# Optimization experiments

Measured on AMD Instinct MI355X. Metric: run time of the kernel, lower is better.

## Reference

```python
import jax, jax.numpy as jnp
import numpy as np

N_GRAPHS = 1000  # fixed num_segments (torch uses batch.max()+1; ids drawn in [0, N_GRAPHS))


def setup_inputs() -> dict:
    key = jax.random.key(0)
    ks = jax.random.split(key, 12)
    n, d, h, e = 100000, 128, 128, 1600000
    x = jax.random.normal(ks[0], (n, d), jnp.float32)
    edge_index = jax.random.randint(ks[1], (2, e), 0, n)
    batch = jnp.sort(jax.random.randint(ks[2], (n,), 0, N_GRAPHS))

    def lin_w(k, i, o):
        return jax.random.normal(k, (i, o), jnp.float32) / np.sqrt(i).astype(np.float32)

    return {
        "x": x, "edge_index": edge_index, "batch": batch,
        "W0": lin_w(ks[3], d, h), "b0": jnp.zeros((h,), jnp.float32),
        "W1": lin_w(ks[4], h, h), "b1": jnp.zeros((h,), jnp.float32),
        "W2": lin_w(ks[5], h, h), "b2": jnp.zeros((h,), jnp.float32),
        "Wp1": lin_w(ks[6], h, h), "bp1": jnp.zeros((h,), jnp.float32),
        "Wp2": lin_w(ks[7], h, 1), "bp2": jnp.zeros((1,), jnp.float32),
    }


def reference(x, edge_index, batch, W0, b0, W1, b1, W2, b2, Wp1, bp1, Wp2, bp2):
    n = x.shape[0]
    src, dst = edge_index[0], edge_index[1]
    loop = jnp.arange(n, dtype=edge_index.dtype)
    src_a = jnp.concatenate([src, loop])  # [E+N]
    dst_a = jnp.concatenate([dst, loop])  # [E+N]

    # degree with self-loops, symmetric GCN norm per edge
    deg = jax.ops.segment_sum(jnp.ones_like(dst_a, dtype=x.dtype), dst_a, num_segments=n)
    dd = deg[src_a] * deg[dst_a]
    norm = jnp.where(dd > 0, jax.lax.rsqrt(dd), jnp.zeros_like(dd))  # [E+N]

    for W, b in ((W0, b0), (W1, b1), (W2, b2)):
        h = x @ W + b                              # [N, H] dense linear
        msg = h[src_a] * norm[:, None]             # gather + scale, [E+N, H]
        out = jax.ops.segment_sum(msg, dst_a, num_segments=n)  # scatter-add
        x = jax.nn.relu(out)

    # segment-mean pool over graphs
    pool = jax.ops.segment_sum(x, batch, num_segments=N_GRAPHS)  # [G, H]
    cnt = jax.ops.segment_sum(jnp.ones((n,), x.dtype), batch, num_segments=N_GRAPHS)
    pool = pool / jnp.clip(cnt, 1.0)[:, None]

    hid = jax.nn.relu(pool @ Wp1 + bp1)
    return (hid @ Wp2 + bp2).squeeze(-1)  # [G]
```

## Files before the change

kernel.cpp:

```cpp
#include <hip/hip_runtime.h>
#include <hip/hip_bf16.h>
#include <math.h>


typedef float f32x4 __attribute__((ext_vector_type(4)));
typedef short s16x8 __attribute__((ext_vector_type(8)));
typedef _Float16 f16;
typedef _Float16 f16x4 __attribute__((ext_vector_type(4)));

__device__ __forceinline__ unsigned short f2bf(float x) {
  unsigned u = __float_as_uint(x);
  unsigned r = (u + 0x7FFFu + ((u >> 16) & 1u)) >> 16;
  return (unsigned short)r;
}

__global__ __launch_bounds__(1024) void tile_reduce_kernel(
    const int* __restrict__ indeg, int* __restrict__ tilesum, int n) {
  __shared__ int ws[16];
  int i = blockIdx.x * 1024 + threadIdx.x;
  int v = (i < n) ? indeg[i] : 0;
  for (int off = 32; off > 0; off >>= 1) v += __shfl_down(v, off);
  int wid = threadIdx.x >> 6, lane = threadIdx.x & 63;
  if (lane == 0) ws[wid] = v;
  __syncthreads();
  if (threadIdx.x == 0) {
    int s = 0;
    for (int w = 0; w < 16; ++w) s += ws[w];
    tilesum[blockIdx.x] = s;
  }
}

__global__ __launch_bounds__(1024) void scan_emit_kernel(
    const int* __restrict__ indeg, const int* __restrict__ tilesum,
    int* __restrict__ ptr, float* __restrict__ rsq, int n, int T) {
  __shared__ int wsum[16];
  __shared__ int tilebase_s;
  int bid = blockIdx.x;
  int lane = threadIdx.x & 63, wid = threadIdx.x >> 6;
  if (threadIdx.x < 64) {
    int acc = 0;
    for (int t = threadIdx.x; t < bid; t += 64) acc += tilesum[t];
    for (int off = 32; off > 0; off >>= 1) acc += __shfl_down(acc, off);
    if (threadIdx.x == 0) tilebase_s = acc;
  }
  __syncthreads();
  int tilebase = tilebase_s;
  int i = bid * 1024 + threadIdx.x;
  int v = (i < n) ? indeg[i] : 0;
  int x = v;
  for (int off = 1; off < 64; off <<= 1) {
    int y = __shfl_up(x, off);
    if (lane >= off) x += y;
  }
  if (lane == 63) wsum[wid] = x;
  __syncthreads();
  if (threadIdx.x == 0) {
    int run = 0;
    for (int w = 0; w < 16; ++w) { int t = wsum[w]; wsum[w] = run; run += t; }
  }
  __syncthreads();
  if (i < n) {
    ptr[i] = x - v + wsum[wid] + tilebase;
    rsq[i] = 1.0f / sqrtf((float)(v + 1));
  }
  if (bid == T - 1 && threadIdx.x == 1023) ptr[n] = tilebase + wsum[15] + x;
}

__device__ __forceinline__ void wsplit_body(
    int blk, const float* __restrict__ W0, const float* __restrict__ W1,
    const float* __restrict__ W2, short* __restrict__ Whi, short* __restrict__ Wlo) {
  int layer = blk >> 6;
  int i = (blk & 63) * 256 + threadIdx.x;
  const float* W = (layer == 0) ? W0 : (layer == 1) ? W1 : W2;
  int j = i & 7, lane = (i >> 3) & 63, ks = (i >> 9) & 3, nt = i >> 11;
  int k = ks * 32 + (lane >> 4) * 8 + j;
  int nn = nt * 16 + (lane & 15);
  float w = W[k * 128 + nn];
  unsigned short h = f2bf(w);
  float hf = __uint_as_float(((unsigned)h) << 16);
  Whi[layer * 16384 + i] = (short)h;
  Wlo[layer * 16384 + i] = (short)f2bf(w - hf);
}

__global__ __launch_bounds__(256) void uber0_kernel(
    const int* __restrict__ dst, int* __restrict__ indeg, int* __restrict__ rank,
    int E,
    const float* __restrict__ W0, const float* __restrict__ W1,
    const float* __restrict__ W2, short* __restrict__ Whi, short* __restrict__ Wlo,
    const int* __restrict__ batch, int* __restrict__ gptr, int n, int G,
    float* __restrict__ pool, int CD, int GBD) {
  int b = blockIdx.x;
  if (b < CD) {
    int e = b * 256 + threadIdx.x;
    if (e < E) rank[e] = atomicAdd(&indeg[dst[e]], 1);
  } else if (b < CD + 192) {
    wsplit_body(b - CD, W0, W1, W2, Whi, Wlo);
  } else if (b < CD + 192 + GBD) {
    int i = (b - CD - 192) * 256 + threadIdx.x;
    if (i < n) {
      int bb = batch[i];
      if (i == 0) {
        for (int g = 0; g <= bb; ++g) gptr[g] = 0;
      } else {
        int bp = batch[i - 1];
        for (int g = bp + 1; g <= bb; ++g) gptr[g] = i;
      }
      if (i == n - 1) {
        for (int g = bb + 1; g <= G; ++g) gptr[g] = n;
      }
    }
  } else {
    int i = (b - CD - 192 - GBD) * 256 + threadIdx.x;
    if (i * 4 < G * 128) ((float4*)pool)[i] = make_float4(0.f, 0.f, 0.f, 0.f);
  }
}

__global__ void fill_all_kernel(const int* __restrict__ src, const int* __restrict__ dst,
                                const int* __restrict__ rank, const int* __restrict__ ptr,
                                int* __restrict__ csrc, int E) {
  int i = blockIdx.x * 256 + threadIdx.x;
  if (i < E) {
    int s = src[i], d = dst[i], r = rank[i];
    csrc[ptr[d] + r] = s;
  }
}

__global__ __launch_bounds__(256) void gemm1_kernel(
    const float* __restrict__ X, const short* __restrict__ Whi,
    const short* __restrict__ Wlo, const float* __restrict__ bias,
    const float* __restrict__ rsq, f16* __restrict__ H, int n) {
  int wave = threadIdx.x >> 6, lane = threadIdx.x & 63;
  int quad = lane >> 4, m = lane & 15;
  int mbase = blockIdx.x * 64 + wave * 16;
  int row = min(mbase + m, n - 1);
  const float* xr = X + (size_t)row * 128 + quad * 8;
  const s16x8* WH = (const s16x8*)Whi;
  const s16x8* WL = (const s16x8*)Wlo;
  f32x4 acc[8];
#pragma unroll
  for (int nt = 0; nt < 8; ++nt) acc[nt] = 0.f;
#pragma unroll
  for (int ks = 0; ks < 4; ++ks) {
    float4 xa = *(const float4*)(xr + ks * 32);
    float4 xb = *(const float4*)(xr + ks * 32 + 4);
    float xs[8] = {xa.x, xa.y, xa.z, xa.w, xb.x, xb.y, xb.z, xb.w};
    s16x8 ah, al;
#pragma unroll
    for (int j = 0; j < 8; ++j) {
      unsigned short h = f2bf(xs[j]);
      float hf = __uint_as_float(((unsigned)h) << 16);
      ah[j] = (short)h;
      al[j] = (short)f2bf(xs[j] - hf);
    }
#pragma unroll
    for (int nt = 0; nt < 8; ++nt) {
      s16x8 wh = WH[(nt * 4 + ks) * 64 + lane];
      s16x8 wl = WL[(nt * 4 + ks) * 64 + lane];
      acc[nt] = __builtin_amdgcn_mfma_f32_16x16x32_bf16(ah, wh, acc[nt], 0, 0, 0);
      acc[nt] = __builtin_amdgcn_mfma_f32_16x16x32_bf16(al, wh, acc[nt], 0, 0, 0);
      acc[nt] = __builtin_amdgcn_mfma_f32_16x16x32_bf16(ah, wl, acc[nt], 0, 0, 0);
    }
  }
  float rs[4];
#pragma unroll
  for (int r = 0; r < 4; ++r) {
    int rr = mbase + quad * 4 + r;
    rs[r] = (rr < n) ? rsq[rr] : 0.f;
  }
#pragma unroll
  for (int nt = 0; nt < 8; ++nt) {
    int col = nt * 16 + m;
    float b = bias[col];
#pragma unroll
    for (int r = 0; r < 4; ++r) {
      int rr = mbase + quad * 4 + r;
      if (rr < n) H[(size_t)rr * 128 + col] = (f16)((acc[nt][r] + b) * rs[r]);
    }
  }
}

__device__ __forceinline__ f32x4 agg_sum(
    const f16* __restrict__ H, const int* __restrict__ ptr,
    const int* __restrict__ csrc, int node, int hl) {
  const char* Hb = (const char*)H;
  unsigned hoff = (unsigned)hl << 3;
  int beg = ptr[node], end = ptr[node + 1];
  f32x4 a = __builtin_convertvector(
      *(const f16x4*)(Hb + (((unsigned)node << 8) | hoff)), f32x4);
#define ROW(s) (*(const f16x4*)(Hb + (((unsigned)(s) << 8) + hoff)))
  for (int base = beg; base < end; base += 32) {
    int m = end - base;
    if (m > 32) m = 32;
    int sl = (hl < m) ? csrc[base + hl] : 0;
    int j = 0;
    for (; j + 15 < m; j += 16) {
      int s0 = __shfl(sl, j + 0, 32), s1 = __shfl(sl, j + 1, 32);
      int s2 = __shfl(sl, j + 2, 32), s3 = __shfl(sl, j + 3, 32);
      int s4 = __shfl(sl, j + 4, 32), s5 = __shfl(sl, j + 5, 32);
      int s6 = __shfl(sl, j + 6, 32), s7 = __shfl(sl, j + 7, 32);
      int s8 = __shfl(sl, j + 8, 32), s9 = __shfl(sl, j + 9, 32);
      int sa = __shfl(sl, j + 10, 32), sb = __shfl(sl, j + 11, 32);
      int sc = __shfl(sl, j + 12, 32), sd = __shfl(sl, j + 13, 32);
      int se = __shfl(sl, j + 14, 32), sf = __shfl(sl, j + 15, 32);
      f16x4 h0 = ROW(s0), h1 = ROW(s1), h2 = ROW(s2), h3 = ROW(s3);
      f16x4 h4 = ROW(s4), h5 = ROW(s5), h6 = ROW(s6), h7 = ROW(s7);
      f16x4 h8 = ROW(s8), h9 = ROW(s9), ha = ROW(sa), hb = ROW(sb);
      f16x4 hc = ROW(sc), hd = ROW(sd), he = ROW(se), hf = ROW(sf);
      f16x4 t0 = ((h0 + h1) + (h2 + h3)) + ((h4 + h5) + (h6 + h7));
      f16x4 t1 = ((h8 + h9) + (ha + hb)) + ((hc + hd) + (he + hf));
      a += __builtin_convertvector(t0, f32x4);
      a += __builtin_convertvector(t1, f32x4);
    }
    for (; j + 7 < m; j += 8) {
      int s0 = __shfl(sl, j + 0, 32), s1 = __shfl(sl, j + 1, 32);
      int s2 = __shfl(sl, j + 2, 32), s3 = __shfl(sl, j + 3, 32);
      int s4 = __shfl(sl, j + 4, 32), s5 = __shfl(sl, j + 5, 32);
      int s6 = __shfl(sl, j + 6, 32), s7 = __shfl(sl, j + 7, 32);
      f16x4 h0 = ROW(s0), h1 = ROW(s1), h2 = ROW(s2), h3 = ROW(s3);
      f16x4 h4 = ROW(s4), h5 = ROW(s5), h6 = ROW(s6), h7 = ROW(s7);
      f16x4 t0 = ((h0 + h1) + (h2 + h3)) + ((h4 + h5) + (h6 + h7));
      a += __builtin_convertvector(t0, f32x4);
    }
    for (; j + 3 < m; j += 4) {
      int s0 = __shfl(sl, j + 0, 32), s1 = __shfl(sl, j + 1, 32);
      int s2 = __shfl(sl, j + 2, 32), s3 = __shfl(sl, j + 3, 32);
      f16x4 t0 = (ROW(s0) + ROW(s1)) + (ROW(s2) + ROW(s3));
      a += __builtin_convertvector(t0, f32x4);
    }
    for (; j < m; ++j) {
      int s0 = __shfl(sl, j, 32);
      a += __builtin_convertvector(ROW(s0), f32x4);
    }
  }
#undef ROW
  return a;
}

#define LDS_STRIDE 132
__global__ __launch_bounds__(256) void agg_gemm_kernel(
    const f16* __restrict__ H, const int* __restrict__ ptr,
    const int* __restrict__ csrc, const float* __restrict__ rsq,
    const short* __restrict__ Whi, const short* __restrict__ Wlo,
    const float* __restrict__ bias, f16* __restrict__ Hout, int n) {
  __shared__ int lds[16 * LDS_STRIDE];
  int hw = threadIdx.x >> 5, hl = threadIdx.x & 31;
  int nbase = blockIdx.x * 16;
#pragma unroll
  for (int rep = 0; rep < 2; ++rep) {
    int nl = hw + rep * 8;
    int node = nbase + nl;
    f32x4 o = 0.f;
    if (node < n) {
      f32x4 s = agg_sum(H, ptr, csrc, node, hl);
      float r = rsq[node];
      o.x = fmaxf(s.x * r, 0.f);
      o.y = fmaxf(s.y * r, 0.f);
      o.z = fmaxf(s.z * r, 0.f);
      o.w = fmaxf(s.w * r, 0.f);
    }
    int* dst = lds + nl * LDS_STRIDE + hl * 4;
#pragma unroll
    for (int c = 0; c < 4; ++c) {
      float v = o[c];
      unsigned short h = f2bf(v);
      float hf = __uint_as_float(((unsigned)h) << 16);
      unsigned short l = f2bf(v - hf);
      dst[c] = (int)((((unsigned)h) << 16) | l);
    }
  }
  __syncthreads();

  int wave = threadIdx.x >> 6, lane = threadIdx.x & 63;
  int quad = lane >> 4, m = lane & 15;
  const s16x8* WH = (const s16x8*)Whi;
  const s16x8* WL = (const s16x8*)Wlo;
  f32x4 acc0 = 0.f, acc1 = 0.f;
  int nt0 = wave * 2, nt1 = wave * 2 + 1;
#pragma unroll
  for (int ks = 0; ks < 4; ++ks) {
    const int* arow = lds + m * LDS_STRIDE + ks * 32 + quad * 8;
    s16x8 ah, al;
#pragma unroll
    for (int j = 0; j < 8; ++j) {
      unsigned p = (unsigned)arow[j];
      ah[j] = (short)(p >> 16);
      al[j] = (short)(p & 0xffffu);
    }
    s16x8 wh0 = WH[(nt0 * 4 + ks) * 64 + lane];
    s16x8 wl0 = WL[(nt0 * 4 + ks) * 64 + lane];
    s16x8 wh1 = WH[(nt1 * 4 + ks) * 64 + lane];
    s16x8 wl1 = WL[(nt1 * 4 + ks) * 64 + lane];
    acc0 = __builtin_amdgcn_mfma_f32_16x16x32_bf16(ah, wh0, acc0, 0, 0, 0);
    acc0 = __builtin_amdgcn_mfma_f32_16x16x32_bf16(al, wh0, acc0, 0, 0, 0);
    acc0 = __builtin_amdgcn_mfma_f32_16x16x32_bf16(ah, wl0, acc0, 0, 0, 0);
    acc1 = __builtin_amdgcn_mfma_f32_16x16x32_bf16(ah, wh1, acc1, 0, 0, 0);
    acc1 = __builtin_amdgcn_mfma_f32_16x16x32_bf16(al, wh1, acc1, 0, 0, 0);
    acc1 = __builtin_amdgcn_mfma_f32_16x16x32_bf16(ah, wl1, acc1, 0, 0, 0);
  }
  float rs[4];
#pragma unroll
  for (int r = 0; r < 4; ++r) {
    int rr = nbase + quad * 4 + r;
    rs[r] = (rr < n) ? rsq[rr] : 0.f;
  }
#pragma unroll
  for (int t = 0; t < 2; ++t) {
    int nt = wave * 2 + t;
    int col = nt * 16 + m;
    float b = bias[col];
    f32x4 a = t ? acc1 : acc0;
#pragma unroll
    for (int r = 0; r < 4; ++r) {
      int rr = nbase + quad * 4 + r;
      if (rr < n) Hout[(size_t)rr * 128 + col] = (f16)((a[r] + b) * rs[r]);
    }
  }
}

__global__ __launch_bounds__(256) void agg_pool_kernel(
    const f16* __restrict__ H, const int* __restrict__ ptr,
    const int* __restrict__ csrc, const float* __restrict__ rsq,
    const int* __restrict__ batch, float* __restrict__ pool, int n) {
  __shared__ float rows[16][128];
  __shared__ int gids[16];
  int hw = threadIdx.x >> 5, hl = threadIdx.x & 31;
  int nbase = blockIdx.x * 16;
#pragma unroll
  for (int rep = 0; rep < 2; ++rep) {
    int nl = hw + rep * 8;
    int node = nbase + nl;
    f32x4 o = 0.f;
    if (node < n) {
      f32x4 s = agg_sum(H, ptr, csrc, node, hl);
      float r = rsq[node];
      o.x = fmaxf(s.x * r, 0.f);
      o.y = fmaxf(s.y * r, 0.f);
      o.z = fmaxf(s.z * r, 0.f);
      o.w = fmaxf(s.w * r, 0.f);
    }
    *(f32x4*)&rows[nl][hl * 4] = o;
    if (hl == 0) gids[nl] = (node < n) ? batch[node] : -1;
  }
  __syncthreads();
  int half = threadIdx.x >> 7;
  int ch = threadIdx.x & 127;
  float acc = 0.f;
  int curg = gids[half * 8];
  for (int i = half * 8; i < half * 8 + 8; ++i) {
    int g = gids[i];
    if (g != curg) {
      if (curg >= 0) atomicAdd(&pool[(size_t)curg * 128 + ch], acc);
      acc = 0.f;
      curg = g;
    }
    if (g >= 0) acc += rows[i][ch];
  }
  if (curg >= 0) atomicAdd(&pool[(size_t)curg * 128 + ch], acc);
}

__global__ __launch_bounds__(128) void head_kernel(
    const float* __restrict__ pool, const int* __restrict__ gptr,
    const float* __restrict__ Wp1, const float* __restrict__ bp1,
    const float* __restrict__ Wp2, const float* __restrict__ bp2,
    float* __restrict__ out, int G) {
  int g = blockIdx.x;
  int j = threadIdx.x;
  __shared__ float ps[128];
  __shared__ float hs[128];
  int cnt = gptr[g + 1] - gptr[g];
  float inv = 1.0f / (float)max(cnt, 1);
  ps[j] = pool[(size_t)g * 128 + j] * inv;
  __syncthreads();
  float acc = bp1[j];
#pragma unroll 8
  for (int k = 0; k < 128; ++k) acc = fmaf(ps[k], Wp1[k * 128 + j], acc);
  hs[j] = fmaxf(acc, 0.f) * Wp2[j];
  __syncthreads();
  for (int off = 64; off > 0; off >>= 1) {
    if (j < off) hs[j] += hs[j + off];
    __syncthreads();
  }
  if (j == 0) out[g] = hs[0] + bp2[0];
}

extern "C" void kernel_launch(void* const* d_in, const int* in_sizes, int n_in,
                              void* d_out, int out_size, void* d_ws, size_t ws_size,
                              hipStream_t stream) {
  const float* x    = (const float*)d_in[0];
  const int*   eidx = (const int*)d_in[1];
  const int*   batch= (const int*)d_in[2];
  const float* W0 = (const float*)d_in[3];
  const float* b0 = (const float*)d_in[4];
  const float* W1 = (const float*)d_in[5];
  const float* b1 = (const float*)d_in[6];
  const float* W2 = (const float*)d_in[7];
  const float* b2 = (const float*)d_in[8];
  const float* Wp1 = (const float*)d_in[9];
  const float* bp1 = (const float*)d_in[10];
  const float* Wp2 = (const float*)d_in[11];
  const float* bp2 = (const float*)d_in[12];
  float* out = (float*)d_out;

  const int N = in_sizes[0] / 128;
  const int E = in_sizes[1] / 2;
  const int G = out_size;
  const int T = (N + 1023) / 1024;

  const int* src = eidx;
  const int* dst = eidx + E;

  char* ws = (char*)d_ws;
  size_t off = 0;
  auto alloc = [&](size_t bytes) -> void* {
    void* p = ws + off;
    off = (off + bytes + 255) & ~(size_t)255;
    return p;
  };
  int*   indeg   = (int*)  alloc((size_t)N * 4);
  int*   ptr     = (int*)  alloc((size_t)(N + 1) * 4);
  float* rsq     = (float*)alloc((size_t)N * 4);
  int*   rank    = (int*)  alloc((size_t)E * 4);
  int*   csrc    = (int*)  alloc((size_t)E * 4);
  f16*   bufA    = (f16*)  alloc((size_t)N * 128 * 2);
  f16*   bufB    = (f16*)  alloc((size_t)N * 128 * 2);
  int*   gptr    = (int*)  alloc((size_t)(G + 1) * 4);
  float* pool    = (float*)alloc((size_t)G * 128 * 4);
  int*   tilesum = (int*)  alloc((size_t)T * 4);
  short* whi     = (short*)alloc(3 * 16384 * 2);
  short* wlo     = (short*)alloc(3 * 16384 * 2);
  (void)ws_size;

  hipMemsetAsync(indeg, 0, (size_t)N * 4, stream);

  const int CD  = (E + 255) / 256;
  const int GBD = (N + 255) / 256;
  const int PZ  = (G * 128 / 4 + 255) / 256;
  uber0_kernel<<<CD + 192 + GBD + PZ, 256, 0, stream>>>(
      dst, indeg, rank, E, W0, W1, W2, whi, wlo, batch, gptr, N, G, pool,
      CD, GBD);

  tile_reduce_kernel<<<T, 1024, 0, stream>>>(indeg, tilesum, N);
  scan_emit_kernel<<<T, 1024, 0, stream>>>(indeg, tilesum, ptr, rsq, N, T);

  fill_all_kernel<<<(E + 255) / 256, 256, 0, stream>>>(src, dst, rank, ptr, csrc, E);
  gemm1_kernel<<<(N + 63) / 64, 256, 0, stream>>>(x, whi, wlo, b0, rsq, bufA, N);

  dim3 fused_grid((N + 15) / 16);
  agg_gemm_kernel<<<fused_grid, 256, 0, stream>>>(bufA, ptr, csrc, rsq,
      whi + 16384, wlo + 16384, b1, bufB, N);
  agg_gemm_kernel<<<fused_grid, 256, 0, stream>>>(bufB, ptr, csrc, rsq,
      whi + 2 * 16384, wlo + 2 * 16384, b2, bufA, N);
  agg_pool_kernel<<<fused_grid, 256, 0, stream>>>(bufA, ptr, csrc, rsq, batch, pool, N);

  head_kernel<<<G, 128, 0, stream>>>(pool, gptr, Wp1, bp1, Wp2, bp2, out, G);
}
```

Measured before the change: 448.6 us.

## Split degree-count atomics across eight copies and fuse CSR fill with first GEMM

The in-degree histogram now uses eight replicated counter arrays chosen by block index. This spreads atomic contention, and the scan turns the per-copy counts into per-copy prefix offsets. The CSR fill kernel is merged with the first-layer GEMM into one launch, which saves a kernel boundary and lets the two run concurrently. The cost is 8x more counter memory to zero and read in the scan and reduce passes, plus the risk of scattered per-copy reads.

```diff
diff --git a/kernel.cpp b/kernel.cpp
--- a/kernel.cpp
+++ b/kernel.cpp
@@ -15,10 +15,14 @@
 }
 
 __global__ __launch_bounds__(1024) void tile_reduce_kernel(
-    const int* __restrict__ indeg, int* __restrict__ tilesum, int n) {
+    const int* __restrict__ cnt8, int* __restrict__ tilesum, int n) {
   __shared__ int ws[16];
   int i = blockIdx.x * 1024 + threadIdx.x;
-  int v = (i < n) ? indeg[i] : 0;
+  int v = 0;
+  if (i < n) {
+#pragma unroll
+    for (int c = 0; c < 8; ++c) v += cnt8[(size_t)c * n + i];
+  }
   for (int off = 32; off > 0; off >>= 1) v += __shfl_down(v, off);
   int wid = threadIdx.x >> 6, lane = threadIdx.x & 63;
   if (lane == 0) ws[wid] = v;
@@ -31,7 +35,7 @@
 }
 
 __global__ __launch_bounds__(1024) void scan_emit_kernel(
-    const int* __restrict__ indeg, const int* __restrict__ tilesum,
+    int* __restrict__ cnt8, const int* __restrict__ tilesum,
     int* __restrict__ ptr, float* __restrict__ rsq, int n, int T) {
   __shared__ int wsum[16];
   __shared__ int tilebase_s;
@@ -46,7 +50,12 @@
   __syncthreads();
   int tilebase = tilebase_s;
   int i = bid * 1024 + threadIdx.x;
-  int v = (i < n) ? indeg[i] : 0;
+  int cc[8];
+  int v = 0;
+  if (i < n) {
+#pragma unroll
+    for (int c = 0; c < 8; ++c) { cc[c] = cnt8[(size_t)c * n + i]; v += cc[c]; }
+  }
   int x = v;
   for (int off = 1; off < 64; off <<= 1) {
     int y = __shfl_up(x, off);
@@ -60,8 +69,15 @@
   }
   __syncthreads();
   if (i < n) {
-    ptr[i] = x - v + wsum[wid] + tilebase;
+    int p = x - v + wsum[wid] + tilebase;
+    ptr[i] = p;
     rsq[i] = 1.0f / sqrtf((float)(v + 1));
+    int run = p;
+#pragma unroll
+    for (int c = 0; c < 8; ++c) {
+      cnt8[(size_t)c * n + i] = run;
+      run += cc[c];
+    }
   }
   if (bid == T - 1 && threadIdx.x == 1023) ptr[n] = tilebase + wsum[15] + x;
 }
@@ -83,7 +99,7 @@
 }
 
 __global__ __launch_bounds__(256) void uber0_kernel(
-    const int* __restrict__ dst, int* __restrict__ indeg, int* __restrict__ rank,
+    const int* __restrict__ dst, int* __restrict__ cnt8, int* __restrict__ rank,
     int E,
     const float* __restrict__ W0, const float* __restrict__ W1,
     const float* __restrict__ W2, short* __restrict__ Whi, short* __restrict__ Wlo,
@@ -92,7 +108,10 @@
   int b = blockIdx.x;
   if (b < CD) {
     int e = b * 256 + threadIdx.x;
-    if (e < E) rank[e] = atomicAdd(&indeg[dst[e]], 1);
+    if (e < E) {
+      int copy = b & 7;
+      rank[e] = atomicAdd(&cnt8[(size_t)copy * n + dst[e]], 1);
+    }
   } else if (b < CD + 192) {
     wsplit_body(b - CD, W0, W1, W2, Whi, Wlo);
   } else if (b < CD + 192 + GBD) {
@@ -115,23 +134,26 @@
   }
 }
 
-__global__ void fill_all_kernel(const int* __restrict__ src, const int* __restrict__ dst,
-                                const int* __restrict__ rank, const int* __restrict__ ptr,
-                                int* __restrict__ csrc, int E) {
-  int i = blockIdx.x * 256 + threadIdx.x;
-  if (i < E) {
-    int s = src[i], d = dst[i], r = rank[i];
-    csrc[ptr[d] + r] = s;
-  }
-}
-
-__global__ __launch_bounds__(256) void gemm1_kernel(
+__global__ __launch_bounds__(256) void fill_gemm1_kernel(
+    const int* __restrict__ src, const int* __restrict__ dst,
+    const int* __restrict__ rank, const int* __restrict__ pref,
+    int* __restrict__ csrc, int E, int FB,
     const float* __restrict__ X, const short* __restrict__ Whi,
     const short* __restrict__ Wlo, const float* __restrict__ bias,
     const float* __restrict__ rsq, f16* __restrict__ H, int n) {
+  int b = blockIdx.x;
+  if (b < FB) {
+    int i = b * 256 + threadIdx.x;
+    if (i < E) {
+      int s = src[i], d = dst[i], r = rank[i];
+      int copy = (b & 7);
+      csrc[pref[(size_t)copy * n + d] + r] = s;
+    }
+    return;
+  }
   int wave = threadIdx.x >> 6, lane = threadIdx.x & 63;
   int quad = lane >> 4, m = lane & 15;
-  int mbase = blockIdx.x * 64 + wave * 16;
+  int mbase = (b - FB) * 64 + wave * 16;
   int row = min(mbase + m, n - 1);
   const float* xr = X + (size_t)row * 128 + quad * 8;
   const s16x8* WH = (const s16x8*)Whi;
@@ -170,11 +192,11 @@
 #pragma unroll
   for (int nt = 0; nt < 8; ++nt) {
     int col = nt * 16 + m;
-    float b = bias[col];
+    float bb = bias[col];
 #pragma unroll
     for (int r = 0; r < 4; ++r) {
       int rr = mbase + quad * 4 + r;
-      if (rr < n) H[(size_t)rr * 128 + col] = (f16)((acc[nt][r] + b) * rs[r]);
+      if (rr < n) H[(size_t)rr * 128 + col] = (f16)((acc[nt][r] + bb) * rs[r]);
     }
   }
 }
@@ -416,7 +438,7 @@
     off = (off + bytes + 255) & ~(size_t)255;
     return p;
   };
-  int*   indeg   = (int*)  alloc((size_t)N * 4);
+  int*   cnt8    = (int*)  alloc((size_t)8 * N * 4);
   int*   ptr     = (int*)  alloc((size_t)(N + 1) * 4);
   float* rsq     = (float*)alloc((size_t)N * 4);
   int*   rank    = (int*)  alloc((size_t)E * 4);
@@ -430,20 +452,22 @@
   short* wlo     = (short*)alloc(3 * 16384 * 2);
   (void)ws_size;
 
-  hipMemsetAsync(indeg, 0, (size_t)N * 4, stream);
+  hipMemsetAsync(cnt8, 0, (size_t)8 * N * 4, stream);
 
   const int CD  = (E + 255) / 256;
   const int GBD = (N + 255) / 256;
   const int PZ  = (G * 128 / 4 + 255) / 256;
   uber0_kernel<<<CD + 192 + GBD + PZ, 256, 0, stream>>>(
-      dst, indeg, rank, E, W0, W1, W2, whi, wlo, batch, gptr, N, G, pool,
+      dst, cnt8, rank, E, W0, W1, W2, whi, wlo, batch, gptr, N, G, pool,
       CD, GBD);
 
-  tile_reduce_kernel<<<T, 1024, 0, stream>>>(indeg, tilesum, N);
-  scan_emit_kernel<<<T, 1024, 0, stream>>>(indeg, tilesum, ptr, rsq, N, T);
-
-  fill_all_kernel<<<(E + 255) / 256, 256, 0, stream>>>(src, dst, rank, ptr, csrc, E);
-  gemm1_kernel<<<(N + 63) / 64, 256, 0, stream>>>(x, whi, wlo, b0, rsq, bufA, N);
+  tile_reduce_kernel<<<T, 1024, 0, stream>>>(cnt8, tilesum, N);
+  scan_emit_kernel<<<T, 1024, 0, stream>>>(cnt8, tilesum, ptr, rsq, N, T);
+
+  const int FB = (E + 255) / 256;
+  const int GB = (N + 63) / 64;
+  fill_gemm1_kernel<<<FB + GB, 256, 0, stream>>>(
+      src, dst, rank, cnt8, csrc, E, FB, x, whi, wlo, b0, rsq, bufA, N);
 
   dim3 fused_grid((N + 15) / 16);
   agg_gemm_kernel<<<fused_grid, 256, 0, stream>>>(bufA, ptr, csrc, rsq,
```

New measurement: 448.5 us. No clear change (-0.0%).
